# Performance work log

Measured on AMD Instinct MI355X. Metric: run time of the kernel, lower is better.

Reference implementation:

```python
import jax, jax.numpy as jnp
import numpy as np

B, T, C = 2, 2048, 2048
H = 16
D = C // H  # head_dim = 128
ROPE_BASE = 10000.0


def rope_cos_sin(seq_len, dim, dtype):
    inv_freq = 1.0 / (ROPE_BASE ** (jnp.arange(0, dim, 2, dtype=jnp.float32) / dim))
    t = jnp.arange(seq_len, dtype=jnp.float32)
    freqs = jnp.outer(t, inv_freq)              # [T, D/2]
    emb = jnp.concatenate([freqs, freqs], -1)   # [T, D]
    return emb.astype(dtype), None  # placeholder replaced below


def rotate_half(x):
    x1, x2 = jnp.split(x, 2, axis=-1)
    return jnp.concatenate([-x2, x1], axis=-1)


def setup_inputs() -> dict:
    key = jax.random.key(0)
    k1, k2, k3 = jax.random.split(key, 3)
    sc = 1.0 / np.sqrt(C)
    x = jax.random.normal(k1, (B, T, C), dtype=jnp.float32)
    w_qkv = jax.random.normal(k2, (C, 3 * C), dtype=jnp.float32) * sc
    w_out = jax.random.normal(k3, (C, C), dtype=jnp.float32) * sc
    return {"x": x, "w_qkv": w_qkv, "w_out": w_out}


def reference(x, w_qkv, w_out):
    Bq, Tq, Cq = x.shape
    qkv = x @ w_qkv                                    # [B,T,3C]
    q, k, v = jnp.split(qkv, 3, axis=-1)
    # [B,T,C] -> [B,H,T,D]
    q = q.reshape(Bq, Tq, H, D).transpose(0, 2, 1, 3)
    k = k.reshape(Bq, Tq, H, D).transpose(0, 2, 1, 3)
    v = v.reshape(Bq, Tq, H, D).transpose(0, 2, 1, 3)
    # RoPE
    inv_freq = 1.0 / (ROPE_BASE ** (jnp.arange(0, D, 2, dtype=jnp.float32) / D))
    freqs = jnp.outer(jnp.arange(Tq, dtype=jnp.float32), inv_freq)  # [T, D/2]
    emb = jnp.concatenate([freqs, freqs], -1)                        # [T, D]
    cos = jnp.cos(emb).astype(x.dtype)[None, None]                   # [1,1,T,D]
    sin = jnp.sin(emb).astype(x.dtype)[None, None]
    q = q * cos + rotate_half(q) * sin
    k = k * cos + rotate_half(k) * sin
    # causal SDPA
    scale = 1.0 / np.sqrt(D)
    att = jnp.einsum("bhqd,bhkd->bhqk", q, k) * scale
    causal = jnp.tril(jnp.ones((Tq, Tq), dtype=bool))
    att = jnp.where(causal[None, None], att, -jnp.inf)
    att = jax.nn.softmax(att, axis=-1)
    y = jnp.einsum("bhqk,bhkd->bhqd", att, v)          # [B,H,T,D]
    y = y.transpose(0, 2, 1, 3).reshape(Bq, Tq, Cq)
    return y @ w_out
```

## Files before the change

### kernel.cpp

```cpp
#include <hip/hip_runtime.h>
#include <hip/hip_bf16.h>
#include <type_traits>
#include <utility>

typedef unsigned short u16;
typedef unsigned int u32;

#define B_ 2
#define T_ 2048
#define C_ 2048
#define H_ 16
#define D_ 128
#define LDQKV 6144

typedef float float4v __attribute__((ext_vector_type(4)));
typedef short short8 __attribute__((ext_vector_type(8)));

__device__ inline u16 f2bf(float f) {
  u32 u = __builtin_bit_cast(u32, f);
  u32 r = u + 0x7fffu + ((u >> 16) & 1u);
  return (u16)(r >> 16);
}
__device__ inline float bfbits2f(u16 b) {
  return __builtin_bit_cast(float, (u32)b << 16);
}

#if defined(__HIP_DEVICE_COMPILE__)
typedef __bf16 bf16x8 __attribute__((ext_vector_type(8)));

template <typename V, typename = void>
struct mfma_takes_short : std::false_type {};
template <typename V>
struct mfma_takes_short<V, std::void_t<decltype(__builtin_amdgcn_mfma_f32_16x16x32_bf16(
    std::declval<V>(), std::declval<V>(), std::declval<float4v>(), 0, 0, 0))>>
    : std::true_type {};

template <typename SV>
__device__ inline float4v mfma_bf16(SV a, SV b, float4v c) {
  if constexpr (mfma_takes_short<SV>::value) {
    return __builtin_amdgcn_mfma_f32_16x16x32_bf16(a, b, c, 0, 0, 0);
  } else {
    return __builtin_amdgcn_mfma_f32_16x16x32_bf16(
        __builtin_bit_cast(bf16x8, a), __builtin_bit_cast(bf16x8, b), c, 0, 0, 0);
  }
}

__device__ inline void async16(u16* lds, const u16* g) {
  typedef __attribute__((address_space(3))) void lds_void;
  typedef __attribute__((address_space(1))) const void g_void;
  __builtin_amdgcn_global_load_lds((g_void*)g, (lds_void*)lds, 16, 0, 0);
}
#endif

__global__ __launch_bounds__(256) void cast_f32_bf16(const float* __restrict__ s,
                                                     u16* __restrict__ d) {
  int i = (blockIdx.x * 256 + threadIdx.x) * 4;
  float4 v = *(const float4*)(s + i);
  alignas(8) u16 o[4] = {f2bf(v.x), f2bf(v.y), f2bf(v.z), f2bf(v.w)};
  *(uint2*)(d + i) = *(const uint2*)o;
}

__global__ __launch_bounds__(256) void castT_f32_bf16(const float* __restrict__ src,
                                                      u16* __restrict__ dst,
                                                      int R, int Cc) {
  __shared__ float tile[32][33];
  const int t = threadIdx.x;
  const int r0 = blockIdx.y * 32, c0 = blockIdx.x * 32;
  const int lr = t >> 3, lc = (t & 7) * 4;
  float4 v = *(const float4*)(src + (size_t)(r0 + lr) * Cc + c0 + lc);
  tile[lr][lc + 0] = v.x;
  tile[lr][lc + 1] = v.y;
  tile[lr][lc + 2] = v.z;
  tile[lr][lc + 3] = v.w;
  __syncthreads();
  alignas(8) u16 o[4];
#pragma unroll
  for (int j = 0; j < 4; ++j) o[j] = f2bf(tile[lc + j][lr]);
  *(uint2*)(dst + (size_t)(c0 + lr) * R + r0 + lc) = *(const uint2*)o;
}

template <bool CF32>
__global__ __launch_bounds__(256) void gemm_bt(const u16* __restrict__ A,
                                               const u16* __restrict__ BT,
                                               void* __restrict__ Cp,
                                               int K, int lda, int ldbt, int ldc) {
#if defined(__HIP_DEVICE_COMPILE__)
  __shared__ u16 As[4096];
  __shared__ u16 Bs[4096];
  const int tid = threadIdx.x;
  const int lane = tid & 63;
  const int w = tid >> 6;
  const int wm = w & 1, wn = w >> 1;
  const int ml = lane & 15, qd = lane >> 4;
  const int m0 = blockIdx.y * 128, n0 = blockIdx.x * 128;
  const int sm = lane >> 2, sk = (lane & 3) * 8;
  const u16* gA[2];
  const u16* gB[2];
  u16 *lA[2], *lB[2];
#pragma unroll
  for (int r = 0; r < 2; ++r) {
    int seg = r * 4 + w;
    gA[r] = A + (size_t)(m0 + seg * 16 + sm) * lda + sk;
    gB[r] = BT + (size_t)(n0 + seg * 16 + sm) * ldbt + sk;
    lA[r] = As + seg * 512;
    lB[r] = Bs + seg * 512;
  }
  float4v acc[4][4] = {};
  for (int kk = 0; kk < K; kk += 32) {
    __syncthreads();
    async16(lA[0], gA[0] + kk);
    async16(lA[1], gA[1] + kk);
    async16(lB[0], gB[0] + kk);
    async16(lB[1], gB[1] + kk);
    __syncthreads();
    short8 a[4], b[4];
#pragma unroll
    for (int mt = 0; mt < 4; ++mt)
      a[mt] = *(const short8*)(As + (wm * 64 + mt * 16 + ml) * 32 + qd * 8);
#pragma unroll
    for (int nt = 0; nt < 4; ++nt)
      b[nt] = *(const short8*)(Bs + (wn * 64 + nt * 16 + ml) * 32 + qd * 8);
#pragma unroll
    for (int mt = 0; mt < 4; ++mt)
#pragma unroll
      for (int nt = 0; nt < 4; ++nt) acc[mt][nt] = mfma_bf16(a[mt], b[nt], acc[mt][nt]);
  }
#pragma unroll
  for (int mt = 0; mt < 4; ++mt) {
#pragma unroll
    for (int nt = 0; nt < 4; ++nt) {
#pragma unroll
      for (int r = 0; r < 4; ++r) {
        int row = m0 + wm * 64 + mt * 16 + qd * 4 + r;
        int col = n0 + wn * 64 + nt * 16 + ml;
        if constexpr (CF32) {
          ((float*)Cp)[(size_t)row * ldc + col] = acc[mt][nt][r];
        } else {
          ((u16*)Cp)[(size_t)row * ldc + col] = f2bf(acc[mt][nt][r]);
        }
      }
    }
  }
#endif
}

template <bool AF32, bool BF32, bool CF32>
__global__ __launch_bounds__(256) void gemm_mixed(const void* __restrict__ Ap,
                                                  const void* __restrict__ Bp,
                                                  void* __restrict__ Cp,
                                                  int M, int N, int K,
                                                  int lda, int ldb, int ldc) {
#if defined(__HIP_DEVICE_COMPILE__)
  __shared__ u16 As[64][40];
  __shared__ u16 Bs[64][40];
  const int tid = threadIdx.x;
  const int lane = tid & 63;
  const int w = tid >> 6;
  const int m0 = blockIdx.y * 64;
  const int n0 = blockIdx.x * 64;
  const int arow = tid >> 2, acol = (tid & 3) * 8;
  const int brow = tid >> 3, bcol = (tid & 7) * 8;
  const int ml = lane & 15, qd = lane >> 4;
  float4v acc[4] = {};
  for (int kk = 0; kk < K; kk += 32) {
    __syncthreads();
    if constexpr (AF32) {
      const float* A = (const float*)Ap;
      const float* src = A + (size_t)(m0 + arow) * lda + (kk + acol);
      float4 f0 = *(const float4*)src;
      float4 f1 = *(const float4*)(src + 4);
      alignas(16) u16 tmp[8] = {f2bf(f0.x), f2bf(f0.y), f2bf(f0.z), f2bf(f0.w),
                                f2bf(f1.x), f2bf(f1.y), f2bf(f1.z), f2bf(f1.w)};
      *(uint4*)(&As[arow][acol]) = *(const uint4*)tmp;
    } else {
      const u16* A = (const u16*)Ap;
      *(uint4*)(&As[arow][acol]) = *(const uint4*)(A + (size_t)(m0 + arow) * lda + (kk + acol));
    }
    if constexpr (BF32) {
      const float* Bm = (const float*)Bp;
      const float* src = Bm + (size_t)(kk + brow) * ldb + (n0 + bcol);
      float4 f0 = *(const float4*)src;
      float4 f1 = *(const float4*)(src + 4);
      float fv[8] = {f0.x, f0.y, f0.z, f0.w, f1.x, f1.y, f1.z, f1.w};
#pragma unroll
      for (int i = 0; i < 8; ++i) Bs[bcol + i][brow] = f2bf(fv[i]);
    } else {
      const u16* Bm = (const u16*)Bp;
      uint4 bv = *(const uint4*)(Bm + (size_t)(kk + brow) * ldb + (n0 + bcol));
      const u16* bsp = (const u16*)&bv;
#pragma unroll
      for (int i = 0; i < 8; ++i) Bs[bcol + i][brow] = bsp[i];
    }
    __syncthreads();
    short8 af = *(const short8*)(&As[w * 16 + ml][qd * 8]);
#pragma unroll
    for (int nt = 0; nt < 4; ++nt) {
      short8 bf = *(const short8*)(&Bs[nt * 16 + ml][qd * 8]);
      acc[nt] = mfma_bf16(af, bf, acc[nt]);
    }
  }
#pragma unroll
  for (int nt = 0; nt < 4; ++nt) {
#pragma unroll
    for (int r = 0; r < 4; ++r) {
      int row = m0 + w * 16 + qd * 4 + r;
      int col = n0 + nt * 16 + ml;
      if constexpr (CF32) {
        ((float*)Cp)[(size_t)row * ldc + col] = acc[nt][r];
      } else {
        ((u16*)Cp)[(size_t)row * ldc + col] = f2bf(acc[nt][r]);
      }
    }
  }
#endif
}

__global__ __launch_bounds__(256) void rope_inplace(u16* __restrict__ qkv) {
  int idx = blockIdx.x * 256 + threadIdx.x;
  int d = idx & 63;
  int h = (idx >> 6) & 15;
  int t = (idx >> 10) & 2047;
  int b = idx >> 21;
  size_t row = (size_t)(b * T_ + t) * LDQKV;
  u16* qp = qkv + row + h * 128;
  u16* kp = qkv + row + C_ + h * 128;
  float q1 = bfbits2f(qp[d]);
  float q2 = bfbits2f(qp[d + 64]);
  float k1 = bfbits2f(kp[d]);
  float k2 = bfbits2f(kp[d + 64]);
  float invf = exp2f((float)d * -0.20762050593046012f);
  float fr = (float)t * invf;
  float sn, cs;
  sincosf(fr, &sn, &cs);
  qp[d] = f2bf(q1 * cs - q2 * sn);
  qp[d + 64] = f2bf(q2 * cs + q1 * sn);
  kp[d] = f2bf(k1 * cs - k2 * sn);
  kp[d + 64] = f2bf(k2 * cs + k1 * sn);
}

__global__ __launch_bounds__(256, 2) void attn_fwd(u16* __restrict__ qkv) {
#if defined(__HIP_DEVICE_COMPILE__)
  __shared__ alignas(16) u16 ks[64][136];
  __shared__ alignas(16) u16 vt[128][72];
  __shared__ alignas(16) u16 pb[4][32][72];
  const int tid = threadIdx.x;
  const int lane = tid & 63;
  const int w = tid >> 6;
  const int ml = lane & 15, qd = lane >> 4;
  const int gx = blockIdx.x;
  const int half = gx >> 8;
  const int rem = gx & 255;
  const int bh = rem >> 3;
  const int q3 = rem & 7;
  const int qt = half ? q3 : (15 - q3);
  const int b = bh >> 4, h = bh & 15;
  const int hc = h * 128;
  const int m0 = qt * 128;
  const size_t rb = (size_t)(b * T_);
  short8 qf[2][4];
#pragma unroll
  for (int m = 0; m < 2; ++m) {
    const u16* qp = qkv + (rb + m0 + w * 32 + m * 16 + ml) * LDQKV + hc;
#pragma unroll
    for (int k4 = 0; k4 < 4; ++k4) qf[m][k4] = *(const short8*)(qp + k4 * 32 + qd * 8);
  }
  float4v acc[2][8] = {};
  float mi[2][4], li[2][4];
#pragma unroll
  for (int m = 0; m < 2; ++m)
#pragma unroll
    for (int r = 0; r < 4; ++r) { mi[m][r] = -1.0e30f; li[m][r] = 0.f; }
  const float scale = 0.08838834764831845f;
  const int srow = tid >> 2;
  const int scol = (tid & 3) * 32;
  const int nchunk = 2 * qt + 2;

  for (int c = 0; c < nchunk; ++c) {
    __syncthreads();
    {
      const u16* kp = qkv + (rb + c * 64 + srow) * LDQKV + C_ + hc + scol;
      const u16* vp = qkv + (rb + c * 64 + srow) * LDQKV + 2 * C_ + hc + scol;
#pragma unroll
      for (int i = 0; i < 4; ++i)
        *(uint4*)&ks[srow][scol + i * 8] = *(const uint4*)(kp + i * 8);
#pragma unroll
      for (int i = 0; i < 4; ++i) {
        uint4 vv = *(const uint4*)(vp + i * 8);
        const u16* e = (const u16*)&vv;
#pragma unroll
        for (int t = 0; t < 8; ++t) vt[scol + i * 8 + t][srow] = e[t];
      }
    }
    __syncthreads();
    if (c * 64 > m0 + w * 32 + 31) continue;
    float4v s[2][4] = {};
#pragma unroll
    for (int t = 0; t < 4; ++t) {
#pragma unroll
      for (int k4 = 0; k4 < 4; ++k4) {
        short8 bf = *(const short8*)(&ks[t * 16 + ml][k4 * 32 + qd * 8]);
        s[0][t] = mfma_bf16(qf[0][k4], bf, s[0][t]);
        s[1][t] = mfma_bf16(qf[1][k4], bf, s[1][t]);
      }
    }
    const bool domask = (c * 64 + 63) > (m0 + w * 32);
#pragma unroll
    for (int m = 0; m < 2; ++m) {
      float al[4];
#pragma unroll
      for (int r = 0; r < 4; ++r) {
        float x0 = s[m][0][r] * scale;
        float x1 = s[m][1][r] * scale;
        float x2 = s[m][2][r] * scale;
        float x3 = s[m][3][r] * scale;
        if (domask) {
          int row = m0 + w * 32 + m * 16 + qd * 4 + r;
          int j0 = c * 64 + ml;
          if (j0 > row) x0 = -1.0e30f;
          if (j0 + 16 > row) x1 = -1.0e30f;
          if (j0 + 32 > row) x2 = -1.0e30f;
          if (j0 + 48 > row) x3 = -1.0e30f;
        }
        float mx = fmaxf(fmaxf(x0, x1), fmaxf(x2, x3));
        mx = fmaxf(mx, __shfl_xor(mx, 1));
        mx = fmaxf(mx, __shfl_xor(mx, 2));
        mx = fmaxf(mx, __shfl_xor(mx, 4));
        mx = fmaxf(mx, __shfl_xor(mx, 8));
        float mnew = fmaxf(mi[m][r], mx);
        float a = __expf(mi[m][r] - mnew);
        float p0 = __expf(x0 - mnew);
        float p1 = __expf(x1 - mnew);
        float p2 = __expf(x2 - mnew);
        float p3 = __expf(x3 - mnew);
        float sm = p0 + p1 + p2 + p3;
        sm += __shfl_xor(sm, 1);
        sm += __shfl_xor(sm, 2);
        sm += __shfl_xor(sm, 4);
        sm += __shfl_xor(sm, 8);
        li[m][r] = li[m][r] * a + sm;
        mi[m][r] = mnew;
        al[r] = a;
        int prow = m * 16 + qd * 4 + r;
        pb[w][prow][ml] = f2bf(p0);
        pb[w][prow][16 + ml] = f2bf(p1);
        pb[w][prow][32 + ml] = f2bf(p2);
        pb[w][prow][48 + ml] = f2bf(p3);
      }
#pragma unroll
      for (int d = 0; d < 8; ++d) {
        acc[m][d][0] *= al[0];
        acc[m][d][1] *= al[1];
        acc[m][d][2] *= al[2];
        acc[m][d][3] *= al[3];
      }
    }
#pragma unroll
    for (int k2 = 0; k2 < 2; ++k2) {
      short8 pa0 = *(const short8*)(&pb[w][ml][k2 * 32 + qd * 8]);
      short8 pa1 = *(const short8*)(&pb[w][16 + ml][k2 * 32 + qd * 8]);
#pragma unroll
      for (int d = 0; d < 8; ++d) {
        short8 vf = *(const short8*)(&vt[d * 16 + ml][k2 * 32 + qd * 8]);
        acc[0][d] = mfma_bf16(pa0, vf, acc[0][d]);
        acc[1][d] = mfma_bf16(pa1, vf, acc[1][d]);
      }
    }
  }
#pragma unroll
  for (int m = 0; m < 2; ++m) {
#pragma unroll
    for (int r = 0; r < 4; ++r) {
      float inv = 1.0f / li[m][r];
      size_t row = rb + m0 + w * 32 + m * 16 + qd * 4 + r;
#pragma unroll
      for (int d = 0; d < 8; ++d)
        qkv[row * LDQKV + hc + d * 16 + ml] = f2bf(acc[m][d][r] * inv);
    }
  }
#endif
}

extern "C" void kernel_launch(void* const* d_in, const int* in_sizes, int n_in,
                              void* d_out, int out_size, void* d_ws, size_t ws_size,
                              hipStream_t stream) {
  const float* x = (const float*)d_in[0];
  const float* wqkv = (const float*)d_in[1];
  const float* wout = (const float*)d_in[2];
  float* out = (float*)d_out;
  char* ws = (char*)d_ws;
  u16* qkv = (u16*)ws;

  const size_t MB = 1024 * 1024;
  if (ws_size >= 96 * MB) {
    u16* xb = (u16*)(ws + 48 * MB);
    u16* wqkvT = (u16*)(ws + 64 * MB);
    u16* woutT = (u16*)(ws + 88 * MB);
    cast_f32_bf16<<<dim3(8192), dim3(256), 0, stream>>>(x, xb);
    castT_f32_bf16<<<dim3(192, 64), dim3(256), 0, stream>>>(wqkv, wqkvT, 2048, 6144);
    castT_f32_bf16<<<dim3(64, 64), dim3(256), 0, stream>>>(wout, woutT, 2048, 2048);
    gemm_bt<false><<<dim3(48, 32), dim3(256), 0, stream>>>(
        xb, wqkvT, qkv, 2048, 2048, 2048, 6144);
    rope_inplace<<<dim3(16384), dim3(256), 0, stream>>>(qkv);
    attn_fwd<<<dim3(512), dim3(256), 0, stream>>>(qkv);
    gemm_bt<true><<<dim3(16, 32), dim3(256), 0, stream>>>(
        qkv, woutT, out, 2048, 6144, 2048, 2048);
  } else {
    gemm_mixed<true, true, false><<<dim3(96, 64), dim3(256), 0, stream>>>(
        x, wqkv, qkv, 4096, 6144, 2048, 2048, 6144, 6144);
    rope_inplace<<<dim3(16384), dim3(256), 0, stream>>>(qkv);
    attn_fwd<<<dim3(512), dim3(256), 0, stream>>>(qkv);
    gemm_mixed<false, true, true><<<dim3(32, 64), dim3(256), 0, stream>>>(
        qkv, wout, out, 4096, 2048, 2048, 6144, 2048, 2048);
  }
}
```

Before: 494.9 us.

## Pre-transpose V and use async swizzled LDS loads in new attention kernel

Adds a separate kernel that writes V transposed per head into workspace, and a new attention kernel that stages K and V^T tiles into LDS with async 16-byte copies using an XOR swizzle. The old path transposed V element by element into shared memory. The softmax scale is folded into Q during RoPE, and P is packed to bf16 two values at a time. In exchange there is an extra launch plus a V^T write and read, and the V^T buffer reuses the wqkvT workspace region after the QKV GEMM has consumed it.

```diff
diff --git a/kernel.cpp b/kernel.cpp
--- a/kernel.cpp
+++ b/kernel.cpp
@@ -23,6 +23,11 @@
 }
 __device__ inline float bfbits2f(u16 b) {
   return __builtin_bit_cast(float, (u32)b << 16);
+}
+__device__ inline u32 pack2bf(float a, float b) {
+  u32 ua = (__builtin_bit_cast(u32, a) + 0x8000u) >> 16;
+  u32 ub = (__builtin_bit_cast(u32, b) + 0x8000u) & 0xffff0000u;
+  return ua | ub;
 }
 
 #if defined(__HIP_DEVICE_COMPILE__)
@@ -77,6 +82,28 @@
 #pragma unroll
   for (int j = 0; j < 4; ++j) o[j] = f2bf(tile[lc + j][lr]);
   *(uint2*)(dst + (size_t)(c0 + lr) * R + r0 + lc) = *(const uint2*)o;
+}
+
+__global__ __launch_bounds__(256) void vT_build(const u16* __restrict__ qkv,
+                                                u16* __restrict__ Vt) {
+  __shared__ u16 lt[64][72];
+  const int tid = threadIdx.x;
+  const int bh = blockIdx.x;
+  const int tt = blockIdx.y;
+  const int dd = blockIdx.z;
+  const int b = bh >> 4, h = bh & 15;
+  const int r = tid >> 2;
+  const int c4 = (tid & 3) * 16;
+  const u16* src = qkv + ((size_t)(b * T_ + tt * 64 + r)) * LDQKV + 2 * C_ + h * 128 + dd * 64 + c4;
+  *(uint4*)&lt[r][c4] = *(const uint4*)src;
+  *(uint4*)&lt[r][c4 + 8] = *(const uint4*)(src + 8);
+  __syncthreads();
+  alignas(16) u16 o[16];
+#pragma unroll
+  for (int j = 0; j < 16; ++j) o[j] = lt[c4 + j][r];
+  u16* dst = Vt + ((size_t)(bh * 128 + dd * 64 + r)) * 2048 + tt * 64 + c4;
+  *(uint4*)dst = *(const uint4*)o;
+  *(uint4*)(dst + 8) = *(const uint4*)(o + 8);
 }
 
 template <bool CF32>
@@ -215,7 +242,7 @@
 #endif
 }
 
-__global__ __launch_bounds__(256) void rope_inplace(u16* __restrict__ qkv) {
+__global__ __launch_bounds__(256) void rope_inplace(u16* __restrict__ qkv, float qscale) {
   int idx = blockIdx.x * 256 + threadIdx.x;
   int d = idx & 63;
   int h = (idx >> 6) & 15;
@@ -232,10 +259,154 @@
   float fr = (float)t * invf;
   float sn, cs;
   sincosf(fr, &sn, &cs);
-  qp[d] = f2bf(q1 * cs - q2 * sn);
-  qp[d + 64] = f2bf(q2 * cs + q1 * sn);
+  qp[d] = f2bf((q1 * cs - q2 * sn) * qscale);
+  qp[d + 64] = f2bf((q2 * cs + q1 * sn) * qscale);
   kp[d] = f2bf(k1 * cs - k2 * sn);
   kp[d + 64] = f2bf(k2 * cs + k1 * sn);
+}
+
+__global__ __launch_bounds__(256, 2) void attn_fwd2(u16* __restrict__ qkv,
+                                                    const u16* __restrict__ Vt) {
+#if defined(__HIP_DEVICE_COMPILE__)
+  __shared__ alignas(16) u16 kS[64 * 128];
+  __shared__ alignas(16) u16 vS[128 * 64];
+  __shared__ alignas(16) u16 pS[4][32][72];
+  const int tid = threadIdx.x;
+  const int lane = tid & 63;
+  const int w = tid >> 6;
+  const int ml = lane & 15, qd = lane >> 4;
+  const int gx = blockIdx.x;
+  const int half = gx >> 8, rem = gx & 255;
+  const int bh = rem >> 3, q3 = rem & 7;
+  const int qt = half ? q3 : (15 - q3);
+  const int b = bh >> 4, h = bh & 15;
+  const int hc = h * 128;
+  const int m0 = qt * 128;
+  const size_t rb = (size_t)(b * T_);
+  short8 qf[2][4];
+#pragma unroll
+  for (int m = 0; m < 2; ++m) {
+    const u16* qp = qkv + (rb + m0 + w * 32 + m * 16 + ml) * LDQKV + hc;
+#pragma unroll
+    for (int k4 = 0; k4 < 4; ++k4) qf[m][k4] = *(const short8*)(qp + k4 * 32 + qd * 8);
+  }
+  float4v acc[2][8] = {};
+  float mi[2] = {-1.0e30f, -1.0e30f}, li[2] = {0.f, 0.f};
+  const int nchunk = 2 * qt + 2;
+  const int krow0 = w * 16 + qd;
+  const int vd0 = w * 32 + (lane >> 3);
+  const int vsegoff = ((lane & 7) ^ (lane >> 3)) * 8;
+  const size_t vtbase = ((size_t)bh * 128) * 2048;
+
+  for (int c = 0; c < nchunk; ++c) {
+    __syncthreads();
+#pragma unroll
+    for (int i = 0; i < 4; ++i) {
+      int key = krow0 + i * 4;
+      int seg = (ml ^ (i * 4 + qd)) * 8;
+      async16(kS + (w * 4 + i) * 512,
+              qkv + (rb + c * 64 + key) * LDQKV + C_ + hc + seg);
+    }
+#pragma unroll
+    for (int i = 0; i < 4; ++i) {
+      int d = vd0 + i * 8;
+      async16(vS + (w * 4 + i) * 512,
+              Vt + vtbase + (size_t)d * 2048 + c * 64 + vsegoff);
+    }
+    __syncthreads();
+    if (c * 64 > m0 + w * 32 + 31) continue;
+    float4v s[4][2] = {};
+#pragma unroll
+    for (int kt = 0; kt < 4; ++kt) {
+#pragma unroll
+      for (int k4 = 0; k4 < 4; ++k4) {
+        int key = kt * 16 + ml;
+        int slot = key * 16 + ((k4 * 4 + qd) ^ key);
+        short8 kf = *(const short8*)(kS + ((kt * 16 + ml) * 16 + ((k4 * 4 + qd) ^ ml)) * 8);
+        (void)key; (void)slot;
+        s[kt][0] = mfma_bf16(kf, qf[0][k4], s[kt][0]);
+        s[kt][1] = mfma_bf16(kf, qf[1][k4], s[kt][1]);
+      }
+    }
+    const bool domask = (c * 64 + 63) > (m0 + w * 32);
+    float alpha[2];
+#pragma unroll
+    for (int m = 0; m < 2; ++m) {
+      int qrow = m0 + w * 32 + m * 16 + ml;
+      if (domask) {
+#pragma unroll
+        for (int kt = 0; kt < 4; ++kt)
+#pragma unroll
+          for (int r = 0; r < 4; ++r) {
+            int key = c * 64 + kt * 16 + qd * 4 + r;
+            if (key > qrow) s[kt][m][r] = -1.0e30f;
+          }
+      }
+      float mx = -1.0e30f;
+#pragma unroll
+      for (int kt = 0; kt < 4; ++kt)
+#pragma unroll
+        for (int r = 0; r < 4; ++r) mx = fmaxf(mx, s[kt][m][r]);
+      mx = fmaxf(mx, __shfl_xor(mx, 16, 64));
+      mx = fmaxf(mx, __shfl_xor(mx, 32, 64));
+      float mnew = fmaxf(mi[m], mx);
+      float a = __expf(mi[m] - mnew);
+      float sm = 0.f;
+#pragma unroll
+      for (int kt = 0; kt < 4; ++kt)
+#pragma unroll
+        for (int r = 0; r < 4; ++r) {
+          float p = __expf(s[kt][m][r] - mnew);
+          s[kt][m][r] = p;
+          sm += p;
+        }
+      sm += __shfl_xor(sm, 16, 64);
+      sm += __shfl_xor(sm, 32, 64);
+      li[m] = li[m] * a + sm;
+      mi[m] = mnew;
+      alpha[m] = a;
+#pragma unroll
+      for (int kt = 0; kt < 4; ++kt) {
+        uint2 pk;
+        pk.x = pack2bf(s[kt][m][0], s[kt][m][1]);
+        pk.y = pack2bf(s[kt][m][2], s[kt][m][3]);
+        *(uint2*)&pS[w][m * 16 + ml][kt * 16 + qd * 4] = pk;
+      }
+    }
+#pragma unroll
+    for (int m = 0; m < 2; ++m) {
+#pragma unroll
+      for (int r = 0; r < 4; ++r) {
+        float aq = __shfl(alpha[m], qd * 4 + r, 64);
+#pragma unroll
+        for (int dt = 0; dt < 8; ++dt) acc[m][dt][r] *= aq;
+      }
+    }
+#pragma unroll
+    for (int k2 = 0; k2 < 2; ++k2) {
+      short8 pa0 = *(const short8*)&pS[w][ml][k2 * 32 + qd * 8];
+      short8 pa1 = *(const short8*)&pS[w][16 + ml][k2 * 32 + qd * 8];
+#pragma unroll
+      for (int dt = 0; dt < 8; ++dt) {
+        int d = dt * 16 + ml;
+        short8 vf = *(const short8*)(vS + (d * 8 + ((k2 * 4 + qd) ^ (ml & 7))) * 8);
+        acc[0][dt] = mfma_bf16(pa0, vf, acc[0][dt]);
+        acc[1][dt] = mfma_bf16(pa1, vf, acc[1][dt]);
+      }
+    }
+  }
+#pragma unroll
+  for (int m = 0; m < 2; ++m) {
+#pragma unroll
+    for (int r = 0; r < 4; ++r) {
+      float inv = 1.0f / __shfl(li[m], qd * 4 + r, 64);
+      size_t row = rb + m0 + w * 32 + m * 16 + qd * 4 + r;
+#pragma unroll
+      for (int dt = 0; dt < 8; ++dt)
+        qkv[row * LDQKV + hc + dt * 16 + ml] = f2bf(acc[m][dt][r] * inv);
+    }
+  }
+#endif
 }
 
 __global__ __launch_bounds__(256, 2) void attn_fwd(u16* __restrict__ qkv) {
@@ -274,7 +445,6 @@
   const int srow = tid >> 2;
   const int scol = (tid & 3) * 32;
   const int nchunk = 2 * qt + 2;
-
   for (int c = 0; c < nchunk; ++c) {
     __syncthreads();
     {
@@ -394,20 +564,22 @@
   if (ws_size >= 96 * MB) {
     u16* xb = (u16*)(ws + 48 * MB);
     u16* wqkvT = (u16*)(ws + 64 * MB);
+    u16* Vt = (u16*)(ws + 64 * MB);
     u16* woutT = (u16*)(ws + 88 * MB);
     cast_f32_bf16<<<dim3(8192), dim3(256), 0, stream>>>(x, xb);
     castT_f32_bf16<<<dim3(192, 64), dim3(256), 0, stream>>>(wqkv, wqkvT, 2048, 6144);
     castT_f32_bf16<<<dim3(64, 64), dim3(256), 0, stream>>>(wout, woutT, 2048, 2048);
     gemm_bt<false><<<dim3(48, 32), dim3(256), 0, stream>>>(
         xb, wqkvT, qkv, 2048, 2048, 2048, 6144);
-    rope_inplace<<<dim3(16384), dim3(256), 0, stream>>>(qkv);
-    attn_fwd<<<dim3(512), dim3(256), 0, stream>>>(qkv);
+    rope_inplace<<<dim3(16384), dim3(256), 0, stream>>>(qkv, 0.08838834764831845f);
+    vT_build<<<dim3(32, 32, 2), dim3(256), 0, stream>>>(qkv, Vt);
+    attn_fwd2<<<dim3(512), dim3(256), 0, stream>>>(qkv, Vt);
     gemm_bt<true><<<dim3(16, 32), dim3(256), 0, stream>>>(
         qkv, woutT, out, 2048, 6144, 2048, 2048);
   } else {
     gemm_mixed<true, true, false><<<dim3(96, 64), dim3(256), 0, stream>>>(
         x, wqkv, qkv, 4096, 6144, 2048, 2048, 6144, 6144);
-    rope_inplace<<<dim3(16384), dim3(256), 0, stream>>>(qkv);
+    rope_inplace<<<dim3(16384), dim3(256), 0, stream>>>(qkv, 1.0f);
     attn_fwd<<<dim3(512), dim3(256), 0, stream>>>(qkv);
     gemm_mixed<false, true, true><<<dim3(32, 64), dim3(256), 0, stream>>>(
         qkv, wout, out, 4096, 2048, 2048, 6144, 2048, 2048);
```

New measurement: 429.4 us. 13.2% less time.
